# Optimization experiments

Measured on AMD Instinct MI355X. Metric: run time of the kernel, lower is better.

Reference implementation:

```python
import jax, jax.numpy as jnp
import numpy as np

N_NODES = 50000


def _mean_aggregate(x, src, dst):
    # gather source features along edges, segment-mean into destinations
    msg = x[src]                                             # [E, d] irregular gather
    agg = jax.ops.segment_sum(msg, dst, num_segments=N_NODES)  # [N, d]
    deg = jax.ops.segment_sum(jnp.ones((src.shape[0],), x.dtype), dst,
                              num_segments=N_NODES)
    return agg / jnp.maximum(deg, 1.0)[:, None]


def setup_inputs() -> dict:
    key = jax.random.key(0)
    ks = jax.random.split(key, 8)
    d_in, d_hid, d_out, L, E = 128, 128, 40, 3, 800000
    s = 1.0 / np.sqrt(d_hid)
    return {
        "x": jax.random.normal(ks[0], (N_NODES, d_in), jnp.float32),
        "edge_index": jax.random.randint(ks[1], (2, E), 0, N_NODES, jnp.int64),
        "Wl": jax.random.normal(ks[2], (L, d_hid, d_hid), jnp.float32) * s,
        "Wr": jax.random.normal(ks[3], (L, d_hid, d_hid), jnp.float32) * s,
        "bl": jnp.zeros((L, d_hid), jnp.float32),
        "W1": jax.random.normal(ks[4], (L * d_hid, d_hid), jnp.float32) * s,
        "b1": jnp.zeros((d_hid,), jnp.float32),
        "W2": jax.random.normal(ks[5], (d_hid, d_out), jnp.float32) * s,
        "b2": jnp.zeros((d_out,), jnp.float32),
    }


def reference(x, edge_index, Wl, Wr, bl, W1, b1, W2, b2):
    src, dst = edge_index[0], edge_index[1]
    h = x
    outs = []
    for i in range(Wl.shape[0]):  # num_layers (structurally small loop)
        m = _mean_aggregate(h, src, dst)          # mean_j x_j  [N, d]
        h = m @ Wl[i] + bl[i] + h @ Wr[i]         # SAGEConv: lin_l(aggr) + lin_r(x)
        outs.append(h)
    z = jnp.concatenate(outs, axis=1)             # [N, L*d]
    z = jax.nn.relu(z @ W1 + b1)
    z = z @ W2 + b2
    return jax.nn.log_softmax(z, axis=1)
```

## Files before the change

kernel.cpp:

```cpp
#include <hip/hip_runtime.h>
#include <math.h>

#define N_NODES 50000
#define D 128
#define LAYERS 3
#define DZ 384
#define DOUT 40
#define BUCKETS 196
#define BR 32

typedef __attribute__((ext_vector_type(4))) float f32x4;
typedef __attribute__((ext_vector_type(8))) short short8;

static __device__ __forceinline__ unsigned short f2bf(float f) {
    unsigned int u = __float_as_uint(f);
    u += 0x7FFFu + ((u >> 16) & 1u);
    return (unsigned short)(u >> 16);
}
static __device__ __forceinline__ float bflo(unsigned int u) {
    return __uint_as_float(u << 16);
}
static __device__ __forceinline__ float bfhi(unsigned int u) {
    return __uint_as_float(u & 0xFFFF0000u);
}
static __device__ __forceinline__ void accq(float* acc, uint4 q, float wgt) {
    acc[0] = fmaf(wgt, bflo(q.x), acc[0]);
    acc[1] = fmaf(wgt, bfhi(q.x), acc[1]);
    acc[2] = fmaf(wgt, bflo(q.y), acc[2]);
    acc[3] = fmaf(wgt, bfhi(q.y), acc[3]);
    acc[4] = fmaf(wgt, bflo(q.z), acc[4]);
    acc[5] = fmaf(wgt, bfhi(q.z), acc[5]);
    acc[6] = fmaf(wgt, bflo(q.w), acc[6]);
    acc[7] = fmaf(wgt, bfhi(q.w), acc[7]);
}


__global__ __launch_bounds__(256) void hist1_kernel(const int* __restrict__ dst, int E, int CH,
                                                    int nblk1, int* __restrict__ H) {
    __shared__ int h[BUCKETS];
    int t = threadIdx.x;
    if (t < BUCKETS) h[t] = 0;
    __syncthreads();
    int s = blockIdx.x * CH, e = min(E, s + CH);
    for (int i = s + t; i < e; i += 256) atomicAdd(&h[dst[i] >> 8], 1);
    __syncthreads();
    if (t < BUCKETS) H[t * nblk1 + blockIdx.x] = h[t];
}

__global__ __launch_bounds__(512) void scanS_kernel(int* __restrict__ H, int nblk1,
                                                    int* __restrict__ T) {
    __shared__ int s[512];
    int t = threadIdx.x, k = blockIdx.x;
    int v = (t < nblk1) ? H[k * nblk1 + t] : 0;
    s[t] = v;
    __syncthreads();
    for (int off = 1; off < 512; off <<= 1) {
        int u = (t >= off) ? s[t - off] : 0;
        __syncthreads();
        s[t] += u;
        __syncthreads();
    }
    if (t < nblk1) H[k * nblk1 + t] = s[t] - v;
    if (t == 511) T[k] = s[511];
}

__global__ __launch_bounds__(256) void bstart_kernel(const int* __restrict__ T,
                                                     int* __restrict__ bucketStart,
                                                     int* __restrict__ offs, int E) {
    __shared__ int s[256];
    int t = threadIdx.x;
    int v = (t < BUCKETS) ? T[t] : 0;
    s[t] = v;
    __syncthreads();
    for (int off = 1; off < 256; off <<= 1) {
        int u = (t >= off) ? s[t - off] : 0;
        __syncthreads();
        s[t] += u;
        __syncthreads();
    }
    if (t < BUCKETS) bucketStart[t] = s[t] - v;
    if (t == 0) { bucketStart[BUCKETS] = E; offs[N_NODES] = E; }
}

__global__ __launch_bounds__(256) void scatter_kernel(const int* __restrict__ src,
                                                      const int* __restrict__ dst, int E, int CH,
                                                      int nblk1, const int* __restrict__ H,
                                                      const int* __restrict__ bucketStart,
                                                      unsigned int* __restrict__ recs) {
    __shared__ int cur[BUCKETS];
    int t = threadIdx.x;
    if (t < BUCKETS) cur[t] = bucketStart[t] + H[t * nblk1 + blockIdx.x];
    __syncthreads();
    int s = blockIdx.x * CH, e = min(E, s + CH);
    for (int i = s + t; i < e; i += 256) {
        int d = dst[i];
        int pos = atomicAdd(&cur[d >> 8], 1);
        recs[pos] = (unsigned int)(src[i] & 0xFFFF) | ((unsigned int)(d & 255) << 16);
    }
}

__global__ __launch_bounds__(256) void bucket_csr_kernel(const unsigned int* __restrict__ recs,
                                                         const int* __restrict__ bucketStart,
                                                         int* __restrict__ offs,
                                                         unsigned short* __restrict__ adj) {
    __shared__ int h[256];
    __shared__ int sc[256];
    __shared__ int cur[256];
    int t = threadIdx.x, k = blockIdx.x;
    int bs = bucketStart[k], be = bucketStart[k + 1];
    h[t] = 0;
    __syncthreads();
    for (int i = bs + t; i < be; i += 256) atomicAdd(&h[(recs[i] >> 16) & 255], 1);
    __syncthreads();
    int v = h[t];
    sc[t] = v;
    __syncthreads();
    for (int off = 1; off < 256; off <<= 1) {
        int u = (t >= off) ? sc[t - off] : 0;
        __syncthreads();
        sc[t] += u;
        __syncthreads();
    }
    int excl = sc[t] - v;
    int node = k * 256 + t;
    if (node < N_NODES) offs[node] = bs + excl;
    cur[t] = bs + excl;
    __syncthreads();
    for (int i = bs + t; i < be; i += 256) {
        unsigned int r = recs[i];
        int pos = atomicAdd(&cur[(r >> 16) & 255], 1);
        adj[pos] = (unsigned short)(r & 0xFFFF);
    }
}


__global__ __launch_bounds__(256) void prep_kernel(const float* __restrict__ x,
                                                   const float* __restrict__ Wl,
                                                   const float* __restrict__ Wr,
                                                   const float* __restrict__ W1,
                                                   const float* __restrict__ W2,
                                                   unsigned short* __restrict__ xb,
                                                   unsigned short* __restrict__ WT,
                                                   unsigned short* __restrict__ W1T,
                                                   unsigned short* __restrict__ W2T,
                                                   int n4) {
    int i = blockIdx.x * blockDim.x + threadIdx.x;
    if (i < n4) {
        const float4 v = ((const float4*)x)[i];
        unsigned int lo = ((unsigned int)f2bf(v.y) << 16) | f2bf(v.x);
        unsigned int hi = ((unsigned int)f2bf(v.w) << 16) | f2bf(v.z);
        ((unsigned int*)xb)[i * 2] = lo;
        ((unsigned int*)xb)[i * 2 + 1] = hi;
        return;
    }
    int j = i - n4;
    if (j < LAYERS * 128 * 256) {
        int layer = j >> 15;
        int r = j & 32767;
        int c = r >> 8, k = r & 255;
        const float* W = (k < 128) ? (Wl + layer * 16384) : (Wr + layer * 16384);
        WT[j] = f2bf(W[(k & 127) * 128 + c]);
        return;
    }
    j -= LAYERS * 128 * 256;
    if (j < 128 * 384) {
        int c = j / 384, k = j - c * 384;
        W1T[j] = f2bf(W1[k * 128 + c]);
        return;
    }
    j -= 128 * 384;
    if (j < 48 * 128) {
        int c = j >> 7, k = j & 127;
        W2T[j] = (c < DOUT) ? f2bf(W2[k * DOUT + c]) : (unsigned short)0;
    }
}

__global__ __launch_bounds__(512) void sage_fused_kernel(
        const unsigned short* __restrict__ h,
        const int* __restrict__ offs, const unsigned short* __restrict__ adj,
        const unsigned short* __restrict__ WT,
        const float* __restrict__ bl,
        unsigned short* __restrict__ zout) {
    __shared__ unsigned short mlds[BR][136];
    __shared__ unsigned short hlds[BR][136];
    int tid = threadIdx.x;
    int r0 = blockIdx.x * BR;
    int gid = tid >> 4, l16 = tid & 15;

    {
        int row = tid >> 4, c8 = (tid & 15) * 8;
        int rc = min(r0 + row, N_NODES - 1);
        *(uint4*)(&hlds[row][c8]) = *(const uint4*)(h + (size_t)rc * D + c8);
    }

    {
        const unsigned short* hb = h + l16 * 8;
        int node = r0 + gid;
        float acc[8];
#pragma unroll
        for (int j = 0; j < 8; ++j) acc[j] = 0.f;
        int s = 0, e = 0;
        if (node < N_NODES) { s = offs[node]; e = offs[node + 1]; }
        for (int k = s; k < e; k += 4) {
            int e1 = e - 1;
            int a0 = adj[k];
            int a1 = adj[min(k + 1, e1)];
            int a2 = adj[min(k + 2, e1)];
            int a3 = adj[min(k + 3, e1)];
            uint4 q0 = *(const uint4*)(hb + (size_t)a0 * D);
            uint4 q1 = *(const uint4*)(hb + (size_t)a1 * D);
            uint4 q2 = *(const uint4*)(hb + (size_t)a2 * D);
            uint4 q3 = *(const uint4*)(hb + (size_t)a3 * D);
            float w1 = (k + 1 < e) ? 1.f : 0.f;
            float w2 = (k + 2 < e) ? 1.f : 0.f;
            float w3 = (k + 3 < e) ? 1.f : 0.f;
            accq(acc, q0, 1.f);
            accq(acc, q1, w1);
            accq(acc, q2, w2);
            accq(acc, q3, w3);
        }
        float inv = 1.f / fmaxf((float)(e - s), 1.f);
        uint4 o;
        o.x = ((unsigned int)f2bf(acc[1] * inv) << 16) | f2bf(acc[0] * inv);
        o.y = ((unsigned int)f2bf(acc[3] * inv) << 16) | f2bf(acc[2] * inv);
        o.z = ((unsigned int)f2bf(acc[5] * inv) << 16) | f2bf(acc[4] * inv);
        o.w = ((unsigned int)f2bf(acc[7] * inv) << 16) | f2bf(acc[6] * inv);
        *(uint4*)(&mlds[gid][l16 * 8]) = o;
    }
    __syncthreads();

    int wid = tid >> 6;
    int lane = tid & 63;
    int lrow = lane & 15;
    int lk8 = (lane >> 4) * 8;
    int colBase = wid * 16;
    f32x4 acc0 = (f32x4){0.f,0.f,0.f,0.f};
    f32x4 acc1 = (f32x4){0.f,0.f,0.f,0.f};

#pragma unroll
    for (int kc = 0; kc < 8; ++kc) {
        short8 aF0, aF1;
        if (kc < 4) {
            aF0 = *(const short8*)(&mlds[lrow][kc * 32 + lk8]);
            aF1 = *(const short8*)(&mlds[16 + lrow][kc * 32 + lk8]);
        } else {
            aF0 = *(const short8*)(&hlds[lrow][(kc - 4) * 32 + lk8]);
            aF1 = *(const short8*)(&hlds[16 + lrow][(kc - 4) * 32 + lk8]);
        }
        short8 bF = *(const short8*)(WT + (size_t)(colBase + lrow) * 256 + kc * 32 + lk8);
        acc0 = __builtin_amdgcn_mfma_f32_16x16x32_bf16(aF0, bF, acc0, 0, 0, 0);
        acc1 = __builtin_amdgcn_mfma_f32_16x16x32_bf16(aF1, bF, acc1, 0, 0, 0);
    }

    int ocol = lane & 15;
    int orow0 = r0 + (lane >> 4) * 4;
    int col = colBase + ocol;
    float b = bl[col];
#pragma unroll
    for (int j = 0; j < 4; ++j) {
        int ra = orow0 + j;
        int rb = ra + 16;
        if (ra < N_NODES) zout[(size_t)ra * D + col] = f2bf(acc0[j] + b);
        if (rb < N_NODES) zout[(size_t)rb * D + col] = f2bf(acc1[j] + b);
    }
}

__global__ __launch_bounds__(512) void mlp_fused_kernel(
        const unsigned short* __restrict__ z0,
        const unsigned short* __restrict__ z1b,
        const unsigned short* __restrict__ z2,
        const unsigned short* __restrict__ W1T,
        const float* __restrict__ b1,
        const unsigned short* __restrict__ W2T,
        const float* __restrict__ b2,
        float* __restrict__ out) {
    __shared__ unsigned short zs[BR][392];
    int tid = threadIdx.x;
    int wid = tid >> 6;
    int lane = tid & 63;
    int r0 = blockIdx.x * BR;
    int lrow = lane & 15;
    int lk8 = (lane >> 4) * 8;
    int colBase = wid * 16;

    short8 bw[12];
#pragma unroll
    for (int kc = 0; kc < 12; ++kc) {
        bw[kc] = *(const short8*)(W1T + (size_t)(colBase + lrow) * DZ + kc * 32 + lk8);
    }

    const unsigned short* zbuf[3] = {z0, z1b, z2};
#pragma unroll
    for (int b = 0; b < 3; ++b) {
        int row = tid >> 4, c8 = (tid & 15) * 8;
        int rc = min(r0 + row, N_NODES - 1);
        *(uint4*)(&zs[row][b * 128 + c8]) = *(const uint4*)(zbuf[b] + (size_t)rc * D + c8);
    }
    __syncthreads();

    f32x4 acc0 = (f32x4){0.f,0.f,0.f,0.f};
    f32x4 acc1 = (f32x4){0.f,0.f,0.f,0.f};
#pragma unroll
    for (int kc = 0; kc < 12; ++kc) {
        short8 aF0 = *(const short8*)(&zs[lrow][kc * 32 + lk8]);
        short8 aF1 = *(const short8*)(&zs[16 + lrow][kc * 32 + lk8]);
        acc0 = __builtin_amdgcn_mfma_f32_16x16x32_bf16(aF0, bw[kc], acc0, 0, 0, 0);
        acc1 = __builtin_amdgcn_mfma_f32_16x16x32_bf16(aF1, bw[kc], acc1, 0, 0, 0);
    }
    __syncthreads();

    int ocol = lane & 15;
    int lrow0 = (lane >> 4) * 4;
    {
        int col = colBase + ocol;
        float b = b1[col];
#pragma unroll
        for (int j = 0; j < 4; ++j) {
            zs[lrow0 + j][col] = f2bf(fmaxf(acc0[j] + b, 0.f));
            zs[16 + lrow0 + j][col] = f2bf(fmaxf(acc1[j] + b, 0.f));
        }
    }
    __syncthreads();

    if (wid < 2) {
        f32x4 acc[3];
#pragma unroll
        for (int t = 0; t < 3; ++t) acc[t] = (f32x4){0.f,0.f,0.f,0.f};
        int lr = wid * 16 + lrow;
#pragma unroll
        for (int kc = 0; kc < 4; ++kc) {
            short8 aF = *(const short8*)(&zs[lr][kc * 32 + lk8]);
#pragma unroll
            for (int ct = 0; ct < 3; ++ct) {
                short8 bF = *(const short8*)(W2T + (size_t)(ct * 16 + lrow) * 128 + kc * 32 + lk8);
                acc[ct] = __builtin_amdgcn_mfma_f32_16x16x32_bf16(aF, bF, acc[ct], 0, 0, 0);
            }
        }

        float b0 = b2[ocol];
        float b1v = b2[16 + ocol];
        float b2v = (ocol < 8) ? b2[32 + ocol] : 0.f;

#pragma unroll
        for (int j = 0; j < 4; ++j) {
            int orow = r0 + wid * 16 + (lane >> 4) * 4 + j;
            float v0 = acc[0][j] + b0;
            float v1 = acc[1][j] + b1v;
            float v2 = (ocol < 8) ? (acc[2][j] + b2v) : -1e30f;
            float mx = fmaxf(fmaxf(v0, v1), v2);
            mx = fmaxf(mx, __shfl_xor(mx, 1));
            mx = fmaxf(mx, __shfl_xor(mx, 2));
            mx = fmaxf(mx, __shfl_xor(mx, 4));
            mx = fmaxf(mx, __shfl_xor(mx, 8));
            float es = expf(v0 - mx) + expf(v1 - mx) + ((ocol < 8) ? expf(v2 - mx) : 0.f);
            es += __shfl_xor(es, 1);
            es += __shfl_xor(es, 2);
            es += __shfl_xor(es, 4);
            es += __shfl_xor(es, 8);
            float ls = logf(es);
            if (orow < N_NODES) {
                out[(size_t)orow * DOUT + ocol] = v0 - mx - ls;
                out[(size_t)orow * DOUT + 16 + ocol] = v1 - mx - ls;
                if (ocol < 8) out[(size_t)orow * DOUT + 32 + ocol] = v2 - mx - ls;
            }
        }
    }
}


extern "C" void kernel_launch(void* const* d_in, const int* in_sizes, int n_in,
                              void* d_out, int out_size, void* d_ws, size_t ws_size,
                              hipStream_t stream) {
    const float* x   = (const float*)d_in[0];
    const int*   ei  = (const int*)d_in[1];
    const float* Wl  = (const float*)d_in[2];
    const float* Wr  = (const float*)d_in[3];
    const float* bl  = (const float*)d_in[4];
    const float* W1  = (const float*)d_in[5];
    const float* b1  = (const float*)d_in[6];
    const float* W2  = (const float*)d_in[7];
    const float* b2  = (const float*)d_in[8];
    float* out = (float*)d_out;

    const int E = in_sizes[1] / 2;
    const int* src = ei;
    const int* dst = ei + E;

    int CH = 2048;
    int nblk1 = (E + CH - 1) / CH;
    if (nblk1 > 512) { CH = ((E + 511) / 512 + 255) & ~255; nblk1 = (E + CH - 1) / CH; }

    char* p = (char*)d_ws;
    auto take = [&p](size_t bytes) { char* q = p; p += (bytes + 255) & ~(size_t)255; return q; };
    int* offs        = (int*)take((N_NODES + 1) * sizeof(int));
    int* H           = (int*)take((size_t)BUCKETS * nblk1 * sizeof(int));
    int* T           = (int*)take(BUCKETS * sizeof(int));
    int* bucketStart = (int*)take((BUCKETS + 1) * sizeof(int));
    unsigned int*   recs = (unsigned int*)take((size_t)E * sizeof(unsigned int));
    unsigned short* adj  = (unsigned short*)take((size_t)E * sizeof(unsigned short));
    unsigned short* xb  = (unsigned short*)take((size_t)N_NODES * D * 2);
    unsigned short* z0  = (unsigned short*)take((size_t)N_NODES * D * 2);
    unsigned short* z1  = (unsigned short*)take((size_t)N_NODES * D * 2);
    unsigned short* z2  = (unsigned short*)take((size_t)N_NODES * D * 2);
    unsigned short* WT  = (unsigned short*)take((size_t)LAYERS * 128 * 256 * 2);
    unsigned short* W1T = (unsigned short*)take((size_t)128 * 384 * 2);
    unsigned short* W2T = (unsigned short*)take((size_t)48 * 128 * 2);

    int n4 = N_NODES * D / 4;
    int prep_total = n4 + LAYERS * 128 * 256 + 128 * 384 + 48 * 128;
    prep_kernel<<<(prep_total + 255) / 256, 256, 0, stream>>>(
        x, Wl, Wr, W1, W2, xb, WT, W1T, W2T, n4);

    hist1_kernel<<<nblk1, 256, 0, stream>>>(dst, E, CH, nblk1, H);
    scanS_kernel<<<BUCKETS, 512, 0, stream>>>(H, nblk1, T);
    bstart_kernel<<<1, 256, 0, stream>>>(T, bucketStart, offs, E);
    scatter_kernel<<<nblk1, 256, 0, stream>>>(src, dst, E, CH, nblk1, H, bucketStart, recs);
    bucket_csr_kernel<<<BUCKETS, 256, 0, stream>>>(recs, bucketStart, offs, adj);

    int fgrid = (N_NODES + BR - 1) / BR;

    unsigned short* zs[3] = {z0, z1, z2};
    for (int i = 0; i < LAYERS; ++i) {
        const unsigned short* hin = (i == 0) ? xb : zs[i - 1];
        sage_fused_kernel<<<fgrid, 512, 0, stream>>>(
            hin, offs, adj, WT + (size_t)i * 128 * 256, bl + (size_t)i * D, zs[i]);
    }

    mlp_fused_kernel<<<fgrid, 512, 0, stream>>>(z0, z1, z2, W1T, b1, W2T, b2, out);
}
```

Before: 197.7 us.

## Pre-sort edges by source bucket before destination CSR build

Adds a first radix-style bucketing pass on source node so that, after the stable second pass by destination bucket, each node's neighbor list is roughly ordered by source. The aim is better gather locality in the three aggregation layers. The cost is four extra kernels and another E-sized record buffer written and read during preprocessing.

```diff
diff --git a/kernel.cpp b/kernel.cpp
--- a/kernel.cpp
+++ b/kernel.cpp
@@ -35,14 +35,26 @@
 }
 
 
-__global__ __launch_bounds__(256) void hist1_kernel(const int* __restrict__ dst, int E, int CH,
+__global__ __launch_bounds__(256) void hist1_kernel(const int* __restrict__ key, int E, int CH,
                                                     int nblk1, int* __restrict__ H) {
     __shared__ int h[BUCKETS];
     int t = threadIdx.x;
     if (t < BUCKETS) h[t] = 0;
     __syncthreads();
     int s = blockIdx.x * CH, e = min(E, s + CH);
-    for (int i = s + t; i < e; i += 256) atomicAdd(&h[dst[i] >> 8], 1);
+    for (int i = s + t; i < e; i += 256) atomicAdd(&h[key[i] >> 8], 1);
+    __syncthreads();
+    if (t < BUCKETS) H[t * nblk1 + blockIdx.x] = h[t];
+}
+
+__global__ __launch_bounds__(256) void histP_kernel(const unsigned int* __restrict__ srecs, int E,
+                                                    int CH, int nblk1, int* __restrict__ H) {
+    __shared__ int h[BUCKETS];
+    int t = threadIdx.x;
+    if (t < BUCKETS) h[t] = 0;
+    __syncthreads();
+    int s = blockIdx.x * CH, e = min(E, s + CH);
+    for (int i = s + t; i < e; i += 256) atomicAdd(&h[srecs[i] >> 24], 1);
     __syncthreads();
     if (t < BUCKETS) H[t * nblk1 + blockIdx.x] = h[t];
 }
@@ -79,23 +91,43 @@
         __syncthreads();
     }
     if (t < BUCKETS) bucketStart[t] = s[t] - v;
-    if (t == 0) { bucketStart[BUCKETS] = E; offs[N_NODES] = E; }
-}
-
-__global__ __launch_bounds__(256) void scatter_kernel(const int* __restrict__ src,
-                                                      const int* __restrict__ dst, int E, int CH,
-                                                      int nblk1, const int* __restrict__ H,
-                                                      const int* __restrict__ bucketStart,
-                                                      unsigned int* __restrict__ recs) {
+    if (t == 0) {
+        bucketStart[BUCKETS] = E;
+        if (offs) offs[N_NODES] = E;
+    }
+}
+
+__global__ __launch_bounds__(256) void scatterS_kernel(const int* __restrict__ src,
+                                                       const int* __restrict__ dst, int E, int CH,
+                                                       int nblk1, const int* __restrict__ HS,
+                                                       const int* __restrict__ bucketStartS,
+                                                       unsigned int* __restrict__ srecs) {
+    __shared__ int cur[BUCKETS];
+    int t = threadIdx.x;
+    if (t < BUCKETS) cur[t] = bucketStartS[t] + HS[t * nblk1 + blockIdx.x];
+    __syncthreads();
+    int s = blockIdx.x * CH, e = min(E, s + CH);
+    for (int i = s + t; i < e; i += 256) {
+        int sv = src[i];
+        int pos = atomicAdd(&cur[sv >> 8], 1);
+        srecs[pos] = (unsigned int)(sv & 0xFFFF) | ((unsigned int)(dst[i] & 0xFFFF) << 16);
+    }
+}
+
+__global__ __launch_bounds__(256) void scatterP_kernel(const unsigned int* __restrict__ srecs,
+                                                       int E, int CH, int nblk1,
+                                                       const int* __restrict__ H,
+                                                       const int* __restrict__ bucketStart,
+                                                       unsigned int* __restrict__ recs) {
     __shared__ int cur[BUCKETS];
     int t = threadIdx.x;
     if (t < BUCKETS) cur[t] = bucketStart[t] + H[t * nblk1 + blockIdx.x];
     __syncthreads();
     int s = blockIdx.x * CH, e = min(E, s + CH);
     for (int i = s + t; i < e; i += 256) {
-        int d = dst[i];
-        int pos = atomicAdd(&cur[d >> 8], 1);
-        recs[pos] = (unsigned int)(src[i] & 0xFFFF) | ((unsigned int)(d & 255) << 16);
+        unsigned int r = srecs[i];
+        int pos = atomicAdd(&cur[r >> 24], 1);
+        recs[pos] = (r & 0xFFFFu) | (((r >> 16) & 255u) << 16);
     }
 }
 
@@ -392,12 +424,16 @@
 
     char* p = (char*)d_ws;
     auto take = [&p](size_t bytes) { char* q = p; p += (bytes + 255) & ~(size_t)255; return q; };
-    int* offs        = (int*)take((N_NODES + 1) * sizeof(int));
-    int* H           = (int*)take((size_t)BUCKETS * nblk1 * sizeof(int));
-    int* T           = (int*)take(BUCKETS * sizeof(int));
-    int* bucketStart = (int*)take((BUCKETS + 1) * sizeof(int));
-    unsigned int*   recs = (unsigned int*)take((size_t)E * sizeof(unsigned int));
-    unsigned short* adj  = (unsigned short*)take((size_t)E * sizeof(unsigned short));
+    int* offs         = (int*)take((N_NODES + 1) * sizeof(int));
+    int* HS           = (int*)take((size_t)BUCKETS * nblk1 * sizeof(int));
+    int* H            = (int*)take((size_t)BUCKETS * nblk1 * sizeof(int));
+    int* TS           = (int*)take(BUCKETS * sizeof(int));
+    int* T            = (int*)take(BUCKETS * sizeof(int));
+    int* bucketStartS = (int*)take((BUCKETS + 1) * sizeof(int));
+    int* bucketStart  = (int*)take((BUCKETS + 1) * sizeof(int));
+    unsigned int*   srecs = (unsigned int*)take((size_t)E * sizeof(unsigned int));
+    unsigned int*   recs  = (unsigned int*)take((size_t)E * sizeof(unsigned int));
+    unsigned short* adj   = (unsigned short*)take((size_t)E * sizeof(unsigned short));
     unsigned short* xb  = (unsigned short*)take((size_t)N_NODES * D * 2);
     unsigned short* z0  = (unsigned short*)take((size_t)N_NODES * D * 2);
     unsigned short* z1  = (unsigned short*)take((size_t)N_NODES * D * 2);
@@ -411,19 +447,24 @@
     prep_kernel<<<(prep_total + 255) / 256, 256, 0, stream>>>(
         x, Wl, Wr, W1, W2, xb, WT, W1T, W2T, n4);
 
-    hist1_kernel<<<nblk1, 256, 0, stream>>>(dst, E, CH, nblk1, H);
+    hist1_kernel<<<nblk1, 256, 0, stream>>>(src, E, CH, nblk1, HS);
+    scanS_kernel<<<BUCKETS, 512, 0, stream>>>(HS, nblk1, TS);
+    bstart_kernel<<<1, 256, 0, stream>>>(TS, bucketStartS, (int*)nullptr, E);
+    scatterS_kernel<<<nblk1, 256, 0, stream>>>(src, dst, E, CH, nblk1, HS, bucketStartS, srecs);
+
+    histP_kernel<<<nblk1, 256, 0, stream>>>(srecs, E, CH, nblk1, H);
     scanS_kernel<<<BUCKETS, 512, 0, stream>>>(H, nblk1, T);
     bstart_kernel<<<1, 256, 0, stream>>>(T, bucketStart, offs, E);
-    scatter_kernel<<<nblk1, 256, 0, stream>>>(src, dst, E, CH, nblk1, H, bucketStart, recs);
+    scatterP_kernel<<<nblk1, 256, 0, stream>>>(srecs, E, CH, nblk1, H, bucketStart, recs);
     bucket_csr_kernel<<<BUCKETS, 256, 0, stream>>>(recs, bucketStart, offs, adj);
 
     int fgrid = (N_NODES + BR - 1) / BR;
 
-    unsigned short* zs[3] = {z0, z1, z2};
+    unsigned short* zsb[3] = {z0, z1, z2};
     for (int i = 0; i < LAYERS; ++i) {
-        const unsigned short* hin = (i == 0) ? xb : zs[i - 1];
+        const unsigned short* hin = (i == 0) ? xb : zsb[i - 1];
         sage_fused_kernel<<<fgrid, 512, 0, stream>>>(
-            hin, offs, adj, WT + (size_t)i * 128 * 256, bl + (size_t)i * D, zs[i]);
+            hin, offs, adj, WT + (size_t)i * 128 * 256, bl + (size_t)i * D, zsb[i]);
     }
 
     mlp_fused_kernel<<<fgrid, 512, 0, stream>>>(z0, z1, z2, W1T, b1, W2T, b2, out);
```

Result: slower. 209.9 us (+6.2%).
